# Optimization experiments

Hardware: AMD Instinct MI355X
Metric: run time of the kernel (lower is better)

Reference implementation:

```python
import jax, jax.numpy as jnp
import numpy as np

MODEL_DIM = 1024
NUM_HEADS = 16
HEAD_DIM = MODEL_DIM // NUM_HEADS
SCALE = HEAD_DIM ** -0.5


def setup_inputs() -> dict:
    key = jax.random.key(0)
    ks = jax.random.split(key, 8)
    B, LQ, LC = 2, 2048, 2048
    # lecun-normal init: std = 1/sqrt(fan_in)
    std = MODEL_DIM ** -0.5
    return {
        "query": jax.random.normal(ks[0], (B, LQ, MODEL_DIM), jnp.float32),
        "context": jax.random.normal(ks[1], (B, LC, MODEL_DIM), jnp.float32),
        "Wq": jax.random.normal(ks[2], (MODEL_DIM, MODEL_DIM), jnp.float32) * std,
        "bq": jnp.zeros((MODEL_DIM,), jnp.float32),
        "Wkv": jax.random.normal(ks[3], (MODEL_DIM, 2 * MODEL_DIM), jnp.float32) * std,
        "bkv": jnp.zeros((2 * MODEL_DIM,), jnp.float32),
        "Wout": jax.random.normal(ks[4], (MODEL_DIM, MODEL_DIM), jnp.float32) * std,
        "bout": jnp.zeros((MODEL_DIM,), jnp.float32),
    }


def reference(query, context, Wq, bq, Wkv, bkv, Wout, bout):
    B, LQ, _ = query.shape
    LC = context.shape[1]
    H, D = NUM_HEADS, HEAD_DIM
    # projections
    q = query @ Wq + bq                      # [B, LQ, M]
    kv = context @ Wkv + bkv                 # [B, LC, 2M]
    # einops 'b s (h d c) -> c b h s d': innermost grouping order is (h, d, c)
    kv = kv.reshape(B, LC, H, D, 2)
    k = jnp.transpose(kv[..., 0], (0, 2, 1, 3))   # [B, H, LC, D]
    v = jnp.transpose(kv[..., 1], (0, 2, 1, 3))   # [B, H, LC, D]
    q = jnp.transpose(q.reshape(B, LQ, H, D), (0, 2, 1, 3))  # [B, H, LQ, D]
    # attention
    scores = jnp.einsum('bhid,bhjd->bhij', q, k) * SCALE      # [B, H, LQ, LC]
    attn = jax.nn.softmax(scores, axis=-1)
    out = jnp.einsum('bhij,bhjd->bhid', attn, v)              # [B, H, LQ, D]
    out = jnp.transpose(out, (0, 2, 1, 3)).reshape(B, LQ, H * D)
    return out @ Wout + bout
```

## Files before the change

### kernel.cpp

```cpp
#include <hip/hip_runtime.h>
#include <hip/hip_bf16.h>
#include <stdint.h>

typedef __bf16 bf16_t;
typedef __bf16 bf16x8 __attribute__((ext_vector_type(8)));
typedef __bf16 bf16x4_t __attribute__((ext_vector_type(4)));
typedef float f32x4 __attribute__((ext_vector_type(4)));
typedef float f32x16 __attribute__((ext_vector_type(16)));
typedef unsigned int u32x4 __attribute__((ext_vector_type(4)));

#define B_   2
#define H_   16
#define D_   64
#define LQ_  2048
#define LC_  2048
#define M_   1024

#define EXP2(x) __builtin_amdgcn_exp2f(x)

__device__ __forceinline__ void gload_lds16(const void* g, void* l) {
  __builtin_amdgcn_global_load_lds((__attribute__((address_space(1))) unsigned int*)(g),
                                   (__attribute__((address_space(3))) unsigned int*)(l),
                                   16, 0, 0);
}

__device__ __forceinline__ unsigned pack2(float a, float b) {
  __bf16 x = (__bf16)a, y = (__bf16)b;
  unsigned short ux = __builtin_bit_cast(unsigned short, x);
  unsigned short uy = __builtin_bit_cast(unsigned short, y);
  return (unsigned)ux | ((unsigned)uy << 16);
}

__global__ void prep_kernel(const float* __restrict__ query, const float* __restrict__ context,
                            bf16_t* __restrict__ queryb, bf16_t* __restrict__ ctxb,
                            const float* __restrict__ Wq, const float* __restrict__ Wkv,
                            const float* __restrict__ Wout,
                            bf16_t* __restrict__ Wq_t, bf16_t* __restrict__ Wkv_t,
                            bf16_t* __restrict__ Wout_t) {
  __shared__ float tile[32][33];
  const int bid = blockIdx.x;
  if (bid < 8192) {
    const int n4each = 4096 * 1024 / 4;
    int i = bid * 256 + threadIdx.x;
    const float* in = (i < n4each) ? query : context;
    bf16_t* out = (i < n4each) ? queryb : ctxb;
    const int j = (i < n4each) ? i : (i - n4each);
    const float4 f = ((const float4*)in)[j];
    bf16x4_t o4;
    o4[0] = (__bf16)f.x; o4[1] = (__bf16)f.y; o4[2] = (__bf16)f.z; o4[3] = (__bf16)f.w;
    ((bf16x4_t*)out)[j] = o4;
    return;
  }
  int tb = bid - 8192;
  const float* in; bf16_t* out; int N, kvperm;
  if (tb < 1024)      { in = Wq;   out = Wq_t;   N = 1024; kvperm = 0; }
  else if (tb < 3072) { tb -= 1024; in = Wkv;  out = Wkv_t;  N = 2048; kvperm = 1; }
  else                { tb -= 3072; in = Wout; out = Wout_t; N = 1024; kvperm = 0; }
  const int K = 1024;
  const int nb = N / 32;
  const int n0 = (tb % nb) * 32, k0 = (tb / nb) * 32;
  const int tx = threadIdx.x & 31, ty = threadIdx.x >> 5;
  #pragma unroll
  for (int r = ty; r < 32; r += 8)
    tile[r][tx] = in[(size_t)(k0 + r) * N + (n0 + tx)];
  __syncthreads();
  #pragma unroll
  for (int r = ty; r < 32; r += 8) {
    const int n = n0 + r;
    const int orow = kvperm ? ((n & ~127) | ((n & 1) << 6) | ((n >> 1) & 63)) : n;
    out[(size_t)orow * K + (k0 + tx)] = (__bf16)tile[tx][r];
  }
}

__global__ __launch_bounds__(256, 5)
void proj_fused_kernel(const bf16_t* __restrict__ Aq, const bf16_t* __restrict__ Akv,
                       const bf16_t* __restrict__ Wq_t, const bf16_t* __restrict__ Wkv_t,
                       const float* __restrict__ bq, const float* __restrict__ bkv,
                       bf16_t* __restrict__ q_s, bf16_t* __restrict__ k_s,
                       bf16_t* __restrict__ v_t) {
  __shared__ __attribute__((aligned(16))) bf16_t ldsA[128 * 64];
  __shared__ __attribute__((aligned(16))) bf16_t ldsB[64 * 64];
  const int tid  = threadIdx.x;
  const int wave = tid >> 6, lane = tid & 63;
  const int bid  = blockIdx.x + 48 * blockIdx.y;
  const int nbid = (bid & 7) * 192 + (bid >> 3);
  const int ny = nbid / 48, nx = nbid % 48;
  const bool isq = (nx < 16);
  const bf16_t* A  = isq ? Aq : Akv;
  const bf16_t* Bt = isq ? Wq_t : Wkv_t;
  const int n0 = (isq ? nx : (nx - 16)) * 64;
  const int m0 = ny * 128;
  const int K  = 1024;
  const int wr = wave >> 1, wc = wave & 1;
  const int lrow = lane & 15, lg = lane >> 4;
  const int srow = lane >> 3;
  const int sc8  = ((lane & 7) ^ srow) * 8;

  f32x4 acc[4][2] = {};

  for (int k0 = 0; k0 < K; k0 += 64) {
    __syncthreads();
    #pragma unroll
    for (int i = 0; i < 4; ++i) {
      const int c = wave * 4 + i;
      gload_lds16(A + (size_t)(m0 + c * 8 + srow) * K + (k0 + sc8), ldsA + c * 512);
    }
    #pragma unroll
    for (int i = 0; i < 2; ++i) {
      const int c = wave * 2 + i;
      gload_lds16(Bt + (size_t)(n0 + c * 8 + srow) * K + (k0 + sc8), ldsB + c * 512);
    }
    __syncthreads();
    #pragma unroll
    for (int ks = 0; ks < 2; ++ks) {
      bf16x8 af[4], bfv[2];
      #pragma unroll
      for (int mi = 0; mi < 4; ++mi)
        af[mi] = *(const bf16x8*)(ldsA + (wr * 64 + mi * 16 + lrow) * 64 +
                                  (((ks * 4 + lg) ^ (lrow & 7)) * 8));
      #pragma unroll
      for (int ni = 0; ni < 2; ++ni)
        bfv[ni] = *(const bf16x8*)(ldsB + (wc * 32 + ni * 16 + lrow) * 64 +
                                   (((ks * 4 + lg) ^ (lrow & 7)) * 8));
      #pragma unroll
      for (int mi = 0; mi < 4; ++mi)
        #pragma unroll
        for (int ni = 0; ni < 2; ++ni)
          acc[mi][ni] = __builtin_amdgcn_mfma_f32_16x16x32_bf16(af[mi], bfv[ni], acc[mi][ni], 0, 0, 0);
    }
  }

  #pragma unroll
  for (int mi = 0; mi < 4; ++mi) {
    const int rbase = m0 + wr * 64 + mi * 16 + lg * 4;
    #pragma unroll
    for (int ni = 0; ni < 2; ++ni) {
      const int col = n0 + wc * 32 + ni * 16 + lrow;
      if (isq) {
        const float bv = bq[col];
        #pragma unroll
        for (int j = 0; j < 4; ++j)
          q_s[(size_t)(rbase + j) * 1024 + col] =
              (__bf16)((acc[mi][ni][j] + bv) * 0.18033688011112042f);
      } else {
        const int hh = col >> 7, cbit = (col >> 6) & 1, d = col & 63;
        const float bv = bkv[hh * 128 + d * 2 + cbit];
        #pragma unroll
        for (int j = 0; j < 4; ++j) {
          const int row = rbase + j;
          const int bi = row >> 11, lc = row & 2047;
          const float val = acc[mi][ni][j] + bv;
          if (cbit == 0)
            k_s[((size_t)(bi * 16 + hh) * 2048 + lc) * 64 + d] = (__bf16)val;
          else
            v_t[(((size_t)(bi * 16 + hh) * 64 + (lc >> 5)) * 64 + d) * 32 + (lc & 31)] = (__bf16)val;
        }
      }
    }
  }
}

__global__ __launch_bounds__(256)
void gemm_out_kernel(const bf16_t* __restrict__ A, const bf16_t* __restrict__ Bt,
                     const float* __restrict__ bias, float* __restrict__ out0) {
  __shared__ __attribute__((aligned(16))) bf16_t ldsA[128 * 64];
  __shared__ __attribute__((aligned(16))) bf16_t ldsB[64 * 64];
  const int tid  = threadIdx.x;
  const int wave = tid >> 6, lane = tid & 63;
  const int bid  = blockIdx.x + 16 * blockIdx.y;
  const int nbid = (bid & 7) * 64 + (bid >> 3);
  const int m0 = (nbid >> 4) * 128, n0 = (nbid & 15) * 64;
  const int K = 1024, N = 1024;
  const int wr = wave >> 1, wc = wave & 1;
  const int lrow = lane & 15, lg = lane >> 4;
  const int srow = lane >> 3;
  const int sc8  = ((lane & 7) ^ srow) * 8;

  f32x4 acc[4][2] = {};

  for (int k0 = 0; k0 < K; k0 += 64) {
    __syncthreads();
    #pragma unroll
    for (int i = 0; i < 4; ++i) {
      const int c = wave * 4 + i;
      gload_lds16(A + (size_t)(m0 + c * 8 + srow) * K + (k0 + sc8), ldsA + c * 512);
    }
    #pragma unroll
    for (int i = 0; i < 2; ++i) {
      const int c = wave * 2 + i;
      gload_lds16(Bt + (size_t)(n0 + c * 8 + srow) * K + (k0 + sc8), ldsB + c * 512);
    }
    __syncthreads();
    #pragma unroll
    for (int ks = 0; ks < 2; ++ks) {
      bf16x8 af[4], bfv[2];
      #pragma unroll
      for (int mi = 0; mi < 4; ++mi)
        af[mi] = *(const bf16x8*)(ldsA + (wr * 64 + mi * 16 + lrow) * 64 +
                                  (((ks * 4 + lg) ^ (lrow & 7)) * 8));
      #pragma unroll
      for (int ni = 0; ni < 2; ++ni)
        bfv[ni] = *(const bf16x8*)(ldsB + (wc * 32 + ni * 16 + lrow) * 64 +
                                   (((ks * 4 + lg) ^ (lrow & 7)) * 8));
      #pragma unroll
      for (int mi = 0; mi < 4; ++mi)
        #pragma unroll
        for (int ni = 0; ni < 2; ++ni)
          acc[mi][ni] = __builtin_amdgcn_mfma_f32_16x16x32_bf16(af[mi], bfv[ni], acc[mi][ni], 0, 0, 0);
    }
  }

  #pragma unroll
  for (int mi = 0; mi < 4; ++mi) {
    const int rbase = m0 + wr * 64 + mi * 16 + lg * 4;
    #pragma unroll
    for (int ni = 0; ni < 2; ++ni) {
      const int col = n0 + wc * 32 + ni * 16 + lrow;
      const float bv = bias[col];
      #pragma unroll
      for (int j = 0; j < 4; ++j)
        out0[(size_t)(rbase + j) * N + col] = acc[mi][ni][j] + bv;
    }
  }
}

__global__ __launch_bounds__(256, 4)
void attn_kernel(const bf16_t* __restrict__ q, const bf16_t* __restrict__ k,
                 const bf16_t* __restrict__ vt, bf16_t* __restrict__ o) {
  __shared__ __attribute__((aligned(16))) bf16_t stage[4][2048];
  __shared__ float Osh[64][32];
  __shared__ float Lsh[4][32];

  const int tid  = threadIdx.x;
  const int wave = tid >> 6, lane = tid & 63;
  const int li = lane & 31, hi = lane >> 5;

  const int bid  = blockIdx.x;
  const int xcd  = bid & 7, slot = bid >> 3;
  const int bh   = xcd * 4 + (slot >> 6);
  const int qt   = slot & 63;
  const int b    = bh >> 4, h = bh & 15;

  bf16x8 qa[4];
  {
    const bf16_t* qp = q + (size_t)(b * LQ_ + qt * 32 + li) * 1024 + h * 64 + hi * 8;
    #pragma unroll
    for (int ks = 0; ks < 4; ++ks) qa[ks] = *(const bf16x8*)(qp + ks * 16);
  }
  asm volatile("s_waitcnt vmcnt(0)" ::: "memory");

  const int kv0 = wave * (LC_ / 4);
  const bf16_t* kbase  = k  + (size_t)bh * LC_ * 64 + (size_t)kv0 * 64;
  const bf16_t* vtbase = vt + ((size_t)bh * 64 + wave * 16) * 2048;

  const size_t koff = (size_t)(lane >> 3) * 64 + (size_t)(((lane & 7) ^ (lane >> 3)) * 8);

  bf16_t* lk = &stage[wave][0];

#define STAGE_K(T) do {                                                          \
    const bf16_t* kc_ = kbase + (size_t)(T) * 2048;                              \
    _Pragma("unroll")                                                            \
    for (int i_ = 0; i_ < 4; ++i_)                                               \
      gload_lds16(kc_ + koff + (size_t)i_ * 512, lk + i_ * 512);                 \
  } while (0)

  f32x16 oacc[2] = {};
  float l_run = 0.f;

  STAGE_K(0);

  #pragma unroll 1
  for (int t = 0; t < 16; ++t) {
    asm volatile("s_waitcnt vmcnt(0)" ::: "memory");
    __builtin_amdgcn_sched_barrier(0);

    bf16x8 vf[2][2];
    {
      const bf16_t* vtile = vtbase + (size_t)t * 2048;
      #pragma unroll
      for (int dt = 0; dt < 2; ++dt)
        #pragma unroll
        for (int ks2 = 0; ks2 < 2; ++ks2)
          vf[dt][ks2] = *(const bf16x8*)(vtile + (dt * 32 + li) * 32 + ks2 * 16 + hi * 8);
    }
    __builtin_amdgcn_sched_barrier(0);

    bf16x8 kf[4];
    #pragma unroll
    for (int ks = 0; ks < 4; ++ks)
      kf[ks] = *(const bf16x8*)(lk + li * 64 + (((hi + ks * 2) ^ (li & 7)) * 8));

    asm volatile("s_waitcnt lgkmcnt(0)" ::: "memory");
    __builtin_amdgcn_sched_barrier(0);

    int t2 = t + 1; if (t2 > 15) t2 = 15;
    STAGE_K(t2);

    f32x16 sacc = {};
    __builtin_amdgcn_s_setprio(1);
    #pragma unroll
    for (int ks = 0; ks < 4; ++ks)
      sacc = __builtin_amdgcn_mfma_f32_32x32x16_bf16(kf[ks], qa[ks], sacc, 0, 0, 0);
    __builtin_amdgcn_s_setprio(0);

    float pv[16]; float ps = 0.f;
    #pragma unroll
    for (int r = 0; r < 16; ++r) { pv[r] = EXP2(sacc[r]); ps += pv[r]; }
    ps += __shfl_xor(ps, 32, 64);
    l_run += ps;

    unsigned pk[8];
    #pragma unroll
    for (int i = 0; i < 8; ++i) pk[i] = pack2(pv[2 * i], pv[2 * i + 1]);

    unsigned w[8];
    #pragma unroll
    for (int g2 = 0; g2 < 2; ++g2) {
      const int bidx = g2 * 4;
      const unsigned a0 = pk[bidx + 0], a1 = pk[bidx + 1];
      const unsigned b0 = pk[bidx + 2], b1 = pk[bidx + 3];
      const unsigned xa0 = __shfl_xor(a0, 32, 64), xa1 = __shfl_xor(a1, 32, 64);
      const unsigned xb0 = __shfl_xor(b0, 32, 64), xb1 = __shfl_xor(b1, 32, 64);
      w[bidx + 0] = hi ? xb0 : a0;
      w[bidx + 1] = hi ? xb1 : a1;
      w[bidx + 2] = hi ? b0  : xa0;
      w[bidx + 3] = hi ? b1  : xa1;
    }
    const u32x4 pw0 = {w[0], w[1], w[2], w[3]};
    const u32x4 pw1 = {w[4], w[5], w[6], w[7]};
    const bf16x8 pb0 = __builtin_bit_cast(bf16x8, pw0);
    const bf16x8 pb1 = __builtin_bit_cast(bf16x8, pw1);

    __builtin_amdgcn_s_setprio(1);
    #pragma unroll
    for (int dt = 0; dt < 2; ++dt) {
      oacc[dt] = __builtin_amdgcn_mfma_f32_32x32x16_bf16(vf[dt][0], pb0, oacc[dt], 0, 0, 0);
      oacc[dt] = __builtin_amdgcn_mfma_f32_32x32x16_bf16(vf[dt][1], pb1, oacc[dt], 0, 0, 0);
    }
    __builtin_amdgcn_s_setprio(0);
  }
#undef STAGE_K

  if (hi == 0) Lsh[wave][li] = l_run;
  __syncthreads();

  #pragma unroll
  for (int ss = 0; ss < 4; ++ss) {
    if (wave == ss) {
      #pragma unroll
      for (int dt = 0; dt < 2; ++dt)
        #pragma unroll
        for (int r = 0; r < 16; ++r) {
          const int d = dt * 32 + (r & 3) + 8 * (r >> 2) + 4 * hi;
          if (ss == 0) Osh[d][li] = oacc[dt][r];
          else         Osh[d][li] += oacc[dt][r];
        }
    }
    __syncthreads();
  }

  const int qq = tid >> 3, c8 = (tid & 7) * 8;
  const float lg = Lsh[0][qq] + Lsh[1][qq] + Lsh[2][qq] + Lsh[3][qq];
  const float rl = 1.f / lg;

  u32x4 ow;
  #pragma unroll
  for (int j = 0; j < 4; ++j)
    ow[j] = pack2(Osh[c8 + 2 * j][qq] * rl, Osh[c8 + 2 * j + 1][qq] * rl);
  *(u32x4*)(o + (size_t)(b * LQ_ + qt * 32 + qq) * 1024 + h * 64 + c8) = ow;
}

extern "C" void kernel_launch(void* const* d_in, const int* in_sizes, int n_in,
                              void* d_out, int out_size, void* d_ws, size_t ws_size,
                              hipStream_t stream) {
  const float* query   = (const float*)d_in[0];
  const float* context = (const float*)d_in[1];
  const float* Wq      = (const float*)d_in[2];
  const float* bq      = (const float*)d_in[3];
  const float* Wkv     = (const float*)d_in[4];
  const float* bkv     = (const float*)d_in[5];
  const float* Wout    = (const float*)d_in[6];
  const float* bout    = (const float*)d_in[7];

  char* p = (char*)d_ws;
  bf16_t* queryb = (bf16_t*)p; p += (size_t)4096 * 1024 * 2;
  bf16_t* ctxb   = (bf16_t*)p; p += (size_t)4096 * 1024 * 2;
  bf16_t* Wq_t   = (bf16_t*)p; p += (size_t)1024 * 1024 * 2;
  bf16_t* Wkv_t  = (bf16_t*)p; p += (size_t)2048 * 1024 * 2;
  bf16_t* Wout_t = (bf16_t*)p; p += (size_t)1024 * 1024 * 2;
  bf16_t* q_s    = (bf16_t*)p; p += (size_t)4096 * 1024 * 2;
  bf16_t* k_s    = (bf16_t*)p; p += (size_t)4096 * 1024 * 2;
  bf16_t* v_t    = (bf16_t*)p; p += (size_t)4096 * 1024 * 2;
  bf16_t* attnb  = (bf16_t*)p; p += (size_t)4096 * 1024 * 2;
  if ((size_t)(p - (char*)d_ws) > ws_size) return;

  prep_kernel<<<12288, 256, 0, stream>>>(query, context, queryb, ctxb,
                                         Wq, Wkv, Wout, Wq_t, Wkv_t, Wout_t);
  proj_fused_kernel<<<dim3(48, 32), 256, 0, stream>>>(queryb, ctxb, Wq_t, Wkv_t,
                                                      bq, bkv, q_s, k_s, v_t);
  attn_kernel<<<dim3(2048), 256, 0, stream>>>(q_s, k_s, v_t, attnb);
  gemm_out_kernel<<<dim3(16, 32), 256, 0, stream>>>(attnb, Wout_t, bout, (float*)d_out);
}
```

Before: 161.7 us.

## Double-buffer LDS in projection GEMMs and halve attention P shuffles

```diff
diff --git a/kernel.cpp b/kernel.cpp
--- a/kernel.cpp
+++ b/kernel.cpp
@@ -72,14 +72,14 @@
   }
 }
 
-__global__ __launch_bounds__(256, 5)
+__global__ __launch_bounds__(256, 3)
 void proj_fused_kernel(const bf16_t* __restrict__ Aq, const bf16_t* __restrict__ Akv,
                        const bf16_t* __restrict__ Wq_t, const bf16_t* __restrict__ Wkv_t,
                        const float* __restrict__ bq, const float* __restrict__ bkv,
                        bf16_t* __restrict__ q_s, bf16_t* __restrict__ k_s,
                        bf16_t* __restrict__ v_t) {
-  __shared__ __attribute__((aligned(16))) bf16_t ldsA[128 * 64];
-  __shared__ __attribute__((aligned(16))) bf16_t ldsB[64 * 64];
+  __shared__ __attribute__((aligned(16))) bf16_t ldsA[2][128 * 64];
+  __shared__ __attribute__((aligned(16))) bf16_t ldsB[2][64 * 64];
   const int tid  = threadIdx.x;
   const int wave = tid >> 6, lane = tid & 63;
   const int bid  = blockIdx.x + 48 * blockIdx.y;
@@ -96,39 +96,65 @@
   const int srow = lane >> 3;
   const int sc8  = ((lane & 7) ^ srow) * 8;
 
+#define PSTAGE(T, BUF) do {                                                      \
+    const int kk_ = (T) * 64;                                                    \
+    _Pragma("unroll")                                                            \
+    for (int i_ = 0; i_ < 4; ++i_) {                                             \
+      const int c_ = wave * 4 + i_;                                              \
+      gload_lds16(A + (size_t)(m0 + c_ * 8 + srow) * K + (kk_ + sc8),            \
+                  ldsA[BUF] + c_ * 512);                                         \
+    }                                                                            \
+    _Pragma("unroll")                                                            \
+    for (int i_ = 0; i_ < 2; ++i_) {                                             \
+      const int c_ = wave * 2 + i_;                                              \
+      gload_lds16(Bt + (size_t)(n0 + c_ * 8 + srow) * K + (kk_ + sc8),           \
+                  ldsB[BUF] + c_ * 512);                                         \
+    }                                                                            \
+  } while (0)
+
   f32x4 acc[4][2] = {};
 
-  for (int k0 = 0; k0 < K; k0 += 64) {
-    __syncthreads();
-    #pragma unroll
-    for (int i = 0; i < 4; ++i) {
-      const int c = wave * 4 + i;
-      gload_lds16(A + (size_t)(m0 + c * 8 + srow) * K + (k0 + sc8), ldsA + c * 512);
-    }
-    #pragma unroll
-    for (int i = 0; i < 2; ++i) {
-      const int c = wave * 2 + i;
-      gload_lds16(Bt + (size_t)(n0 + c * 8 + srow) * K + (k0 + sc8), ldsB + c * 512);
-    }
-    __syncthreads();
+  PSTAGE(0, 0);
+  asm volatile("s_waitcnt vmcnt(0)" ::: "memory");
+  __builtin_amdgcn_s_barrier();
+  PSTAGE(1, 1);
+
+  #pragma unroll 1
+  for (int kt = 0; kt < 16; ++kt) {
+    const int buf = kt & 1;
+    bf16x8 af[2][4], bfv[2][2];
     #pragma unroll
     for (int ks = 0; ks < 2; ++ks) {
-      bf16x8 af[4], bfv[2];
       #pragma unroll
       for (int mi = 0; mi < 4; ++mi)
-        af[mi] = *(const bf16x8*)(ldsA + (wr * 64 + mi * 16 + lrow) * 64 +
-                                  (((ks * 4 + lg) ^ (lrow & 7)) * 8));
+        af[ks][mi] = *(const bf16x8*)(ldsA[buf] + (wr * 64 + mi * 16 + lrow) * 64 +
+                                      (((ks * 4 + lg) ^ (lrow & 7)) * 8));
       #pragma unroll
       for (int ni = 0; ni < 2; ++ni)
-        bfv[ni] = *(const bf16x8*)(ldsB + (wc * 32 + ni * 16 + lrow) * 64 +
-                                   (((ks * 4 + lg) ^ (lrow & 7)) * 8));
+        bfv[ks][ni] = *(const bf16x8*)(ldsB[buf] + (wc * 32 + ni * 16 + lrow) * 64 +
+                                       (((ks * 4 + lg) ^ (lrow & 7)) * 8));
+    }
+    asm volatile("s_waitcnt lgkmcnt(0)" ::: "memory");
+    __builtin_amdgcn_sched_barrier(0);
+    __builtin_amdgcn_s_barrier();
+
+    int t2 = kt + 2; if (t2 > 15) t2 = 15;
+    PSTAGE(t2, buf);
+
+    #pragma unroll
+    for (int ks = 0; ks < 2; ++ks)
       #pragma unroll
       for (int mi = 0; mi < 4; ++mi)
         #pragma unroll
         for (int ni = 0; ni < 2; ++ni)
-          acc[mi][ni] = __builtin_amdgcn_mfma_f32_16x16x32_bf16(af[mi], bfv[ni], acc[mi][ni], 0, 0, 0);
-    }
-  }
+          acc[mi][ni] = __builtin_amdgcn_mfma_f32_16x16x32_bf16(af[ks][mi], bfv[ks][ni],
+                                                                acc[mi][ni], 0, 0, 0);
+
+    asm volatile("s_waitcnt vmcnt(6)" ::: "memory");
+    __builtin_amdgcn_sched_barrier(0);
+    __builtin_amdgcn_s_barrier();
+  }
+#undef PSTAGE
 
   #pragma unroll
   for (int mi = 0; mi < 4; ++mi) {
@@ -160,11 +186,11 @@
   }
 }
 
-__global__ __launch_bounds__(256)
+__global__ __launch_bounds__(256, 3)
 void gemm_out_kernel(const bf16_t* __restrict__ A, const bf16_t* __restrict__ Bt,
                      const float* __restrict__ bias, float* __restrict__ out0) {
-  __shared__ __attribute__((aligned(16))) bf16_t ldsA[128 * 64];
-  __shared__ __attribute__((aligned(16))) bf16_t ldsB[64 * 64];
+  __shared__ __attribute__((aligned(16))) bf16_t ldsA[2][128 * 64];
+  __shared__ __attribute__((aligned(16))) bf16_t ldsB[2][64 * 64];
   const int tid  = threadIdx.x;
   const int wave = tid >> 6, lane = tid & 63;
   const int bid  = blockIdx.x + 16 * blockIdx.y;
@@ -176,39 +202,65 @@
   const int srow = lane >> 3;
   const int sc8  = ((lane & 7) ^ srow) * 8;
 
+#define OSTAGE(T, BUF) do {                                                      \
+    const int kk_ = (T) * 64;                                                    \
+    _Pragma("unroll")                                                            \
+    for (int i_ = 0; i_ < 4; ++i_) {                                             \
+      const int c_ = wave * 4 + i_;                                              \
+      gload_lds16(A + (size_t)(m0 + c_ * 8 + srow) * K + (kk_ + sc8),            \
+                  ldsA[BUF] + c_ * 512);                                         \
+    }                                                                            \
+    _Pragma("unroll")                                                            \
+    for (int i_ = 0; i_ < 2; ++i_) {                                             \
+      const int c_ = wave * 2 + i_;                                              \
+      gload_lds16(Bt + (size_t)(n0 + c_ * 8 + srow) * K + (kk_ + sc8),           \
+                  ldsB[BUF] + c_ * 512);                                         \
+    }                                                                            \
+  } while (0)
+
   f32x4 acc[4][2] = {};
 
-  for (int k0 = 0; k0 < K; k0 += 64) {
-    __syncthreads();
-    #pragma unroll
-    for (int i = 0; i < 4; ++i) {
-      const int c = wave * 4 + i;
-      gload_lds16(A + (size_t)(m0 + c * 8 + srow) * K + (k0 + sc8), ldsA + c * 512);
-    }
-    #pragma unroll
-    for (int i = 0; i < 2; ++i) {
-      const int c = wave * 2 + i;
-      gload_lds16(Bt + (size_t)(n0 + c * 8 + srow) * K + (k0 + sc8), ldsB + c * 512);
-    }
-    __syncthreads();
+  OSTAGE(0, 0);
+  asm volatile("s_waitcnt vmcnt(0)" ::: "memory");
+  __builtin_amdgcn_s_barrier();
+  OSTAGE(1, 1);
+
+  #pragma unroll 1
+  for (int kt = 0; kt < 16; ++kt) {
+    const int buf = kt & 1;
+    bf16x8 af[2][4], bfv[2][2];
     #pragma unroll
     for (int ks = 0; ks < 2; ++ks) {
-      bf16x8 af[4], bfv[2];
       #pragma unroll
       for (int mi = 0; mi < 4; ++mi)
-        af[mi] = *(const bf16x8*)(ldsA + (wr * 64 + mi * 16 + lrow) * 64 +
-                                  (((ks * 4 + lg) ^ (lrow & 7)) * 8));
+        af[ks][mi] = *(const bf16x8*)(ldsA[buf] + (wr * 64 + mi * 16 + lrow) * 64 +
+                                      (((ks * 4 + lg) ^ (lrow & 7)) * 8));
       #pragma unroll
       for (int ni = 0; ni < 2; ++ni)
-        bfv[ni] = *(const bf16x8*)(ldsB + (wc * 32 + ni * 16 + lrow) * 64 +
-                                   (((ks * 4 + lg) ^ (lrow & 7)) * 8));
+        bfv[ks][ni] = *(const bf16x8*)(ldsB[buf] + (wc * 32 + ni * 16 + lrow) * 64 +
+                                       (((ks * 4 + lg) ^ (lrow & 7)) * 8));
+    }
+    asm volatile("s_waitcnt lgkmcnt(0)" ::: "memory");
+    __builtin_amdgcn_sched_barrier(0);
+    __builtin_amdgcn_s_barrier();
+
+    int t2 = kt + 2; if (t2 > 15) t2 = 15;
+    OSTAGE(t2, buf);
+
+    #pragma unroll
+    for (int ks = 0; ks < 2; ++ks)
       #pragma unroll
       for (int mi = 0; mi < 4; ++mi)
         #pragma unroll
         for (int ni = 0; ni < 2; ++ni)
-          acc[mi][ni] = __builtin_amdgcn_mfma_f32_16x16x32_bf16(af[mi], bfv[ni], acc[mi][ni], 0, 0, 0);
-    }
-  }
+          acc[mi][ni] = __builtin_amdgcn_mfma_f32_16x16x32_bf16(af[ks][mi], bfv[ks][ni],
+                                                                acc[mi][ni], 0, 0, 0);
+
+    asm volatile("s_waitcnt vmcnt(6)" ::: "memory");
+    __builtin_amdgcn_sched_barrier(0);
+    __builtin_amdgcn_s_barrier();
+  }
+#undef OSTAGE
 
   #pragma unroll
   for (int mi = 0; mi < 4; ++mi) {
@@ -316,15 +368,15 @@
     unsigned w[8];
     #pragma unroll
     for (int g2 = 0; g2 < 2; ++g2) {
-      const int bidx = g2 * 4;
-      const unsigned a0 = pk[bidx + 0], a1 = pk[bidx + 1];
-      const unsigned b0 = pk[bidx + 2], b1 = pk[bidx + 3];
-      const unsigned xa0 = __shfl_xor(a0, 32, 64), xa1 = __shfl_xor(a1, 32, 64);
-      const unsigned xb0 = __shfl_xor(b0, 32, 64), xb1 = __shfl_xor(b1, 32, 64);
-      w[bidx + 0] = hi ? xb0 : a0;
-      w[bidx + 1] = hi ? xb1 : a1;
-      w[bidx + 2] = hi ? b0  : xa0;
-      w[bidx + 3] = hi ? b1  : xa1;
+      const int bx = g2 * 4;
+      #pragma unroll
+      for (int ii = 0; ii < 2; ++ii) {
+        const unsigned lo = pk[bx + ii], hi2 = pk[bx + 2 + ii];
+        const unsigned s  = hi ? lo : hi2;
+        const unsigned xs = __shfl_xor(s, 32, 64);
+        w[bx + ii]     = hi ? xs  : lo;
+        w[bx + 2 + ii] = hi ? hi2 : xs;
+      }
     }
     const u32x4 pw0 = {w[0], w[1], w[2], w[3]};
     const u32x4 pw1 = {w[4], w[5], w[6], w[7]};
```

After: 149.7 us. 1.08x faster.
